# Kernel optimization log

Hardware: AMD Instinct MI355X
Metric: run time of the kernel (lower is better)

## Reference

```python
import jax, jax.numpy as jnp
import numpy as np

D_MODEL = 1792
BB = 256
I = D_MODEL + BB  # inner_dim = 2048


def setup_inputs() -> dict:
    key = jax.random.key(0)
    ks = jax.random.split(key, 10)
    s = 1.0 / np.sqrt(I)  # PyTorch LSTM default init range
    u = lambda k, shape: jax.random.uniform(k, shape, jnp.float32, -s, s)
    return {
        "x": jax.random.normal(ks[0], (6, D_MODEL), jnp.float32),
        "y": jax.random.normal(ks[1], (5, BB), jnp.float32),
        "Wih5": u(ks[2], (5, 4 * I, I)),
        "Whh5": u(ks[3], (5, 4 * I, I)),
        "bih5": u(ks[4], (5, 4 * I)),
        "bhh5": u(ks[5], (5, 4 * I)),
        "WihF": u(ks[6], (4 * I, D_MODEL)),
        "WhhF": u(ks[7], (4 * I, I)),
        "bihF": u(ks[8], (4 * I,)),
        "bhhF": u(ks[9], (4 * I,)),
    }


def _cell(h, c, xt, Wih, Whh, bih, bhh):
    # PyTorch LSTM cell: gates in i, f, g, o order
    g = Wih @ xt + bih + Whh @ h + bhh  # (4I,)
    i, f, gg, o = jnp.split(g, 4)
    c = jax.nn.sigmoid(f) * c + jax.nn.sigmoid(i) * jnp.tanh(gg)
    h = jax.nn.sigmoid(o) * jnp.tanh(c)
    return h, c


def reference(x, y, Wih5, Whh5, bih5, bhh5, WihF, WhhF, bihF, bhhF):
    # inpt: (5, inner_dim) = concat of first 5 frames and 5 gts
    inpt = jnp.concatenate([x[:-1], y], axis=1)
    h0 = jnp.zeros((I,), x.dtype)
    c0 = jnp.zeros((I,), x.dtype)

    def step(carry, xs):
        h, c = carry
        xt, Wih, Whh, bih, bhh = xs
        return _cell(h, c, xt, Wih, Whh, bih, bhh), None

    # 5 sequential single-step LSTM cells (distinct weights), fused via scan
    (h, c), _ = jax.lax.scan(step, (h0, c0), (inpt, Wih5, Whh5, bih5, bhh5))
    # final LSTM consumes the last frame (d_model input)
    h, c = _cell(h, c, x[-1], WihF, WhhF, bihF, bhhF)
    return h[-BB:]
```

## Files before the change

kernel.cpp:

```cpp
#include <hip/hip_runtime.h>
#include <cmath>

#define D_MODEL 1792
#define BB      256
#define II      2048
#define FOURI   8192

__device__ __forceinline__ float sigm(float v) { return 1.0f / (1.0f + expf(-v)); }

__device__ __forceinline__ float waveReduce(float s) {
    #pragma unroll
    for (int off = 32; off > 0; off >>= 1) s += __shfl_down(s, off, 64);
    return s;
}

__device__ __forceinline__ void stage2048(float* dst, const float* src, int tid) {
    float4* d4 = (float4*)dst;
    const float4* s4 = (const float4*)src;
    d4[tid]       = s4[tid];
    d4[tid + 256] = s4[tid + 256];
    __syncthreads();
}

__device__ __forceinline__ void stageConcat(float* dst, const float* xt,
                                            const float* yt, int tid) {
    float4* d4 = (float4*)dst;
    const float4* x4 = (const float4*)xt;
    const float4* y4 = (const float4*)yt;
    int i = tid;
    d4[i] = (i < 448) ? x4[i] : y4[i - 448];
    i = tid + 256;
    d4[i] = (i < 448) ? x4[i] : y4[i - 448];
    __syncthreads();
}

__device__ __forceinline__ float dotLds(const float* __restrict__ w,
                                        const float* hs, int lane) {
    float s = 0.f;
    #pragma unroll
    for (int p = 0; p < 8; ++p) {
        const int j = p * 256 + lane * 4;
        float4 a = *(const float4*)(w + j);
        float4 b = *(const float4*)(hs + j);
        s += a.x * b.x + a.y * b.y + a.z * b.z + a.w * b.w;
    }
    return s;
}

__global__ __launch_bounds__(256) void k0(
    const float* __restrict__ x, const float* __restrict__ y,
    const float* __restrict__ Wih5,
    const float* __restrict__ bih5, const float* __restrict__ bhh5,
    float* __restrict__ h0, float* __restrict__ c0, float* __restrict__ gih1)
{
    __shared__ float buf[II];
    __shared__ float partial[4];
    const int tid = threadIdx.x, wave = tid >> 6, lane = tid & 63;
    const int b = blockIdx.x;

    if (b < II) {
        stageConcat(buf, x, y, tid);
        if (wave != 1) {
            const float* wr = Wih5 + ((size_t)wave * II + b) * (size_t)II;
            float s = dotLds(wr, buf, lane);
            s = waveReduce(s);
            if (lane == 0)
                partial[wave] = s + bih5[wave * II + b] + bhh5[wave * II + b];
        } else {
            const float* wr = Wih5 + ((size_t)FOURI + b) * (size_t)II;
            const float* xt = x + D_MODEL;
            const float* yt = y + BB;
            float s = 0.f;
            #pragma unroll
            for (int p = 0; p < 8; ++p) {
                const int j = p * 256 + lane * 4;
                float4 a = *(const float4*)(wr + j);
                float4 v = (p < 7) ? *(const float4*)(xt + j)
                                   : *(const float4*)(yt + (j - D_MODEL));
                s += a.x * v.x + a.y * v.y + a.z * v.z + a.w * v.w;
            }
            s = waveReduce(s);
            if (lane == 0)
                gih1[b] = s + bih5[FOURI + b] + bhh5[FOURI + b];
        }
        __syncthreads();
        if (tid == 0) {
            const float cc = sigm(partial[0]) * tanhf(partial[2]);
            c0[b] = cc;
            h0[b] = sigm(partial[3]) * tanhf(cc);
        }
    } else {
        stageConcat(buf, x + D_MODEL, y + BB, tid);
        const int row = II + (b - II) * 4 + wave;
        const float* wr = Wih5 + ((size_t)FOURI + row) * (size_t)II;
        float s = dotLds(wr, buf, lane);
        s = waveReduce(s);
        if (lane == 0)
            gih1[row] = s + bih5[FOURI + row] + bhh5[FOURI + row];
    }
}

__global__ __launch_bounds__(256) void kmid(
    const float* __restrict__ Whh,
    const float* __restrict__ gih_t,
    const float* __restrict__ h_in, float* __restrict__ h_out,
    float* __restrict__ c,
    const float* __restrict__ WihN,
    const float* __restrict__ bihN, const float* __restrict__ bhhN,
    const float* __restrict__ xN, const float* __restrict__ yN,
    float* __restrict__ gihN)
{
    __shared__ float buf[II];
    __shared__ float partial[4];
    const int tid = threadIdx.x, wave = tid >> 6, lane = tid & 63;
    const int b = blockIdx.x;

    if (b < II) {
        stage2048(buf, h_in, tid);
        const float* wr = Whh + ((size_t)wave * II + b) * (size_t)II;
        float s = dotLds(wr, buf, lane);
        s = waveReduce(s);
        if (lane == 0) partial[wave] = s + gih_t[wave * II + b];
        __syncthreads();
        if (tid == 0) {
            const float cc = sigm(partial[1]) * c[b]
                           + sigm(partial[0]) * tanhf(partial[2]);
            c[b] = cc;
            h_out[b] = sigm(partial[3]) * tanhf(cc);
        }
    } else {
        stageConcat(buf, xN, yN, tid);
        const int row = (b - II) * 4 + wave;
        const float* wr = WihN + (size_t)row * (size_t)II;
        float s = dotLds(wr, buf, lane);
        s = waveReduce(s);
        if (lane == 0) gihN[row] = s + bihN[row] + bhhN[row];
    }
}

__global__ __launch_bounds__(256) void k4(
    const float* __restrict__ Whh4, const float* __restrict__ gih4,
    const float* __restrict__ h_in, float* __restrict__ h_out,
    float* __restrict__ c,
    const float* __restrict__ WihF, const float* __restrict__ bihF,
    const float* __restrict__ bhhF, const float* __restrict__ x5,
    float* __restrict__ gihF)
{
    __shared__ float buf[II];
    __shared__ float partial[4];
    const int tid = threadIdx.x, wave = tid >> 6, lane = tid & 63;
    const int b = blockIdx.x;

    if (b < II) {
        stage2048(buf, h_in, tid);
        const float* wr = Whh4 + ((size_t)wave * II + b) * (size_t)II;
        float s = dotLds(wr, buf, lane);
        s = waveReduce(s);
        if (lane == 0) partial[wave] = s + gih4[wave * II + b];
        __syncthreads();
        if (tid == 0) {
            const float cc = sigm(partial[1]) * c[b]
                           + sigm(partial[0]) * tanhf(partial[2]);
            c[b] = cc;
            h_out[b] = sigm(partial[3]) * tanhf(cc);
        }
    } else {
        float4* d4 = (float4*)buf;
        const float4* s4 = (const float4*)x5;
        d4[tid] = (tid < 448) ? s4[tid] : make_float4(0.f, 0.f, 0.f, 0.f);
        if (tid < 192) d4[tid + 256] = s4[tid + 256];
        __syncthreads();
        const int j = (b - II) * 4 + wave;
        const int row = (j >> 8) * II + D_MODEL + (j & 255);
        const float* wr = WihF + (size_t)row * (size_t)D_MODEL;
        float s = 0.f;
        #pragma unroll
        for (int p = 0; p < 7; ++p) {
            const int jj = p * 256 + lane * 4;
            float4 a = *(const float4*)(wr + jj);
            float4 v = *(const float4*)(buf + jj);
            s += a.x * v.x + a.y * v.y + a.z * v.z + a.w * v.w;
        }
        s = waveReduce(s);
        if (lane == 0) gihF[j] = s + bihF[row] + bhhF[row];
    }
}

__global__ __launch_bounds__(256) void k5(
    const float* __restrict__ WhhF, const float* __restrict__ gihF,
    const float* __restrict__ h_in, const float* __restrict__ c,
    float* __restrict__ out)
{
    __shared__ float buf[II];
    __shared__ float partial[4];
    const int tid = threadIdx.x, wave = tid >> 6, lane = tid & 63;
    const int b = blockIdx.x;

    stage2048(buf, h_in, tid);
    const int r = D_MODEL + b;
    const float* wr = WhhF + ((size_t)wave * II + r) * (size_t)II;
    float s = dotLds(wr, buf, lane);
    s = waveReduce(s);
    if (lane == 0) partial[wave] = s + gihF[wave * BB + b];
    __syncthreads();
    if (tid == 0) {
        const float cc = sigm(partial[1]) * c[r]
                       + sigm(partial[0]) * tanhf(partial[2]);
        out[b] = sigm(partial[3]) * tanhf(cc);
    }
}

extern "C" void kernel_launch(void* const* d_in, const int* in_sizes, int n_in,
                              void* d_out, int out_size, void* d_ws, size_t ws_size,
                              hipStream_t stream) {
    const float* x    = (const float*)d_in[0];
    const float* y    = (const float*)d_in[1];
    const float* Wih5 = (const float*)d_in[2];
    const float* Whh5 = (const float*)d_in[3];
    const float* bih5 = (const float*)d_in[4];
    const float* bhh5 = (const float*)d_in[5];
    const float* WihF = (const float*)d_in[6];
    const float* WhhF = (const float*)d_in[7];
    const float* bihF = (const float*)d_in[8];
    const float* bhhF = (const float*)d_in[9];
    float* out = (float*)d_out;

    float* ws   = (float*)d_ws;
    float* gihA = ws;
    float* gihB = gihA + FOURI;
    float* gihF = gihB + FOURI;
    float* hA   = gihF + 1024;
    float* hB   = hA + II;
    float* cbuf = hB + II;

    const size_t WOFF = (size_t)FOURI * II;

    k0<<<3584, 256, 0, stream>>>(x, y, Wih5, bih5, bhh5, hA, cbuf, gihA);

    kmid<<<4096, 256, 0, stream>>>(
        Whh5 + 1 * WOFF, gihA, hA, hB, cbuf,
        Wih5 + 2 * WOFF, bih5 + 2 * FOURI, bhh5 + 2 * FOURI,
        x + 2 * D_MODEL, y + 2 * BB, gihB);

    kmid<<<4096, 256, 0, stream>>>(
        Whh5 + 2 * WOFF, gihB, hB, hA, cbuf,
        Wih5 + 3 * WOFF, bih5 + 3 * FOURI, bhh5 + 3 * FOURI,
        x + 3 * D_MODEL, y + 3 * BB, gihA);

    kmid<<<4096, 256, 0, stream>>>(
        Whh5 + 3 * WOFF, gihA, hA, hB, cbuf,
        Wih5 + 4 * WOFF, bih5 + 4 * FOURI, bhh5 + 4 * FOURI,
        x + 4 * D_MODEL, y + 4 * BB, gihB);

    k4<<<2304, 256, 0, stream>>>(
        Whh5 + 4 * WOFF, gihB, hB, hA, cbuf,
        WihF, bihF, bhhF, x + 5 * D_MODEL, gihF);

    k5<<<BB, 256, 0, stream>>>(WhhF, gihF, hA, cbuf, out);
}
```

Before: 122.3 us.

## Drop LDS staging of vectors and merge next-step Wih rows into recurrent blocks

Vector operands (h, x/y concat) are now read directly from global memory instead of being staged into shared memory with a barrier, so the 8 KB LDS buffer goes away. Each block now does both its recurrent Whh gate rows and four Wih rows for the next step, which halves the grid to 2048 blocks per kernel. Each block does more work in exchange for fewer blocks and less LDS. The vector reads now go through the cache once per wave rather than once per block.

Measured after the change: 120.1 us. Within noise of the previous version (-1.8%).

```diff
diff --git a/kernel.cpp b/kernel.cpp
--- a/kernel.cpp
+++ b/kernel.cpp
@@ -5,6 +5,7 @@
 #define BB      256
 #define II      2048
 #define FOURI   8192
+#define G       2048
 
 __device__ __forceinline__ float sigm(float v) { return 1.0f / (1.0f + expf(-v)); }
 
@@ -14,93 +15,70 @@
     return s;
 }
 
-__device__ __forceinline__ void stage2048(float* dst, const float* src, int tid) {
-    float4* d4 = (float4*)dst;
-    const float4* s4 = (const float4*)src;
-    d4[tid]       = s4[tid];
-    d4[tid + 256] = s4[tid + 256];
-    __syncthreads();
-}
-
-__device__ __forceinline__ void stageConcat(float* dst, const float* xt,
-                                            const float* yt, int tid) {
-    float4* d4 = (float4*)dst;
-    const float4* x4 = (const float4*)xt;
-    const float4* y4 = (const float4*)yt;
-    int i = tid;
-    d4[i] = (i < 448) ? x4[i] : y4[i - 448];
-    i = tid + 256;
-    d4[i] = (i < 448) ? x4[i] : y4[i - 448];
-    __syncthreads();
-}
-
-__device__ __forceinline__ float dotLds(const float* __restrict__ w,
-                                        const float* hs, int lane) {
+__device__ __forceinline__ float dotG(const float* __restrict__ w,
+                                      const float* __restrict__ v, int lane) {
     float s = 0.f;
     #pragma unroll
     for (int p = 0; p < 8; ++p) {
         const int j = p * 256 + lane * 4;
         float4 a = *(const float4*)(w + j);
-        float4 b = *(const float4*)(hs + j);
+        float4 b = *(const float4*)(v + j);
         s += a.x * b.x + a.y * b.y + a.z * b.z + a.w * b.w;
     }
     return s;
 }
 
-__global__ __launch_bounds__(256) void k0(
+__device__ __forceinline__ float dotConcat(const float* __restrict__ w,
+                                           const float* __restrict__ xt,
+                                           const float* __restrict__ yt,
+                                           int lane) {
+    float s = 0.f;
+    #pragma unroll
+    for (int p = 0; p < 8; ++p) {
+        const int j = p * 256 + lane * 4;
+        float4 a = *(const float4*)(w + j);
+        float4 b = (p < 7) ? *(const float4*)(xt + j)
+                           : *(const float4*)(yt + (j - D_MODEL));
+        s += a.x * b.x + a.y * b.y + a.z * b.z + a.w * b.w;
+    }
+    return s;
+}
+
+__global__ __launch_bounds__(256) void k_first(
     const float* __restrict__ x, const float* __restrict__ y,
     const float* __restrict__ Wih5,
     const float* __restrict__ bih5, const float* __restrict__ bhh5,
     float* __restrict__ h0, float* __restrict__ c0, float* __restrict__ gih1)
 {
-    __shared__ float buf[II];
-    __shared__ float partial[4];
-    const int tid = threadIdx.x, wave = tid >> 6, lane = tid & 63;
-    const int b = blockIdx.x;
-
-    if (b < II) {
-        stageConcat(buf, x, y, tid);
-        if (wave != 1) {
-            const float* wr = Wih5 + ((size_t)wave * II + b) * (size_t)II;
-            float s = dotLds(wr, buf, lane);
-            s = waveReduce(s);
-            if (lane == 0)
-                partial[wave] = s + bih5[wave * II + b] + bhh5[wave * II + b];
-        } else {
-            const float* wr = Wih5 + ((size_t)FOURI + b) * (size_t)II;
-            const float* xt = x + D_MODEL;
-            const float* yt = y + BB;
-            float s = 0.f;
-            #pragma unroll
-            for (int p = 0; p < 8; ++p) {
-                const int j = p * 256 + lane * 4;
-                float4 a = *(const float4*)(wr + j);
-                float4 v = (p < 7) ? *(const float4*)(xt + j)
-                                   : *(const float4*)(yt + (j - D_MODEL));
-                s += a.x * v.x + a.y * v.y + a.z * v.z + a.w * v.w;
-            }
-            s = waveReduce(s);
-            if (lane == 0)
-                gih1[b] = s + bih5[FOURI + b] + bhh5[FOURI + b];
-        }
-        __syncthreads();
-        if (tid == 0) {
-            const float cc = sigm(partial[0]) * tanhf(partial[2]);
-            c0[b] = cc;
-            h0[b] = sigm(partial[3]) * tanhf(cc);
-        }
-    } else {
-        stageConcat(buf, x + D_MODEL, y + BB, tid);
-        const int row = II + (b - II) * 4 + wave;
+    __shared__ float partial[4];
+    const int tid = threadIdx.x, wave = tid >> 6, lane = tid & 63;
+    const int b = blockIdx.x;
+
+    if (wave != 1) {
+        const float* wr = Wih5 + ((size_t)wave * II + b) * (size_t)II;
+        float s = dotConcat(wr, x, y, lane);
+        s = waveReduce(s);
+        if (lane == 0)
+            partial[wave] = s + bih5[wave * II + b] + bhh5[wave * II + b];
+    }
+    __syncthreads();
+    if (tid == 0) {
+        const float cc = sigm(partial[0]) * tanhf(partial[2]);
+        c0[b] = cc;
+        h0[b] = sigm(partial[3]) * tanhf(cc);
+    }
+
+    {
+        const int row = b * 4 + wave;
         const float* wr = Wih5 + ((size_t)FOURI + row) * (size_t)II;
-        float s = dotLds(wr, buf, lane);
+        float s = dotConcat(wr, x + D_MODEL, y + BB, lane);
         s = waveReduce(s);
         if (lane == 0)
             gih1[row] = s + bih5[FOURI + row] + bhh5[FOURI + row];
     }
 }
 
-__global__ __launch_bounds__(256) void kmid(
+__global__ __launch_bounds__(256) void k_mid(
     const float* __restrict__ Whh,
     const float* __restrict__ gih_t,
     const float* __restrict__ h_in, float* __restrict__ h_out,
@@ -110,29 +88,28 @@
     const float* __restrict__ xN, const float* __restrict__ yN,
     float* __restrict__ gihN)
 {
-    __shared__ float buf[II];
-    __shared__ float partial[4];
-    const int tid = threadIdx.x, wave = tid >> 6, lane = tid & 63;
-    const int b = blockIdx.x;
-
-    if (b < II) {
-        stage2048(buf, h_in, tid);
+    __shared__ float partial[4];
+    const int tid = threadIdx.x, wave = tid >> 6, lane = tid & 63;
+    const int b = blockIdx.x;
+
+    {
         const float* wr = Whh + ((size_t)wave * II + b) * (size_t)II;
-        float s = dotLds(wr, buf, lane);
+        float s = dotG(wr, h_in, lane);
         s = waveReduce(s);
         if (lane == 0) partial[wave] = s + gih_t[wave * II + b];
-        __syncthreads();
-        if (tid == 0) {
-            const float cc = sigm(partial[1]) * c[b]
-                           + sigm(partial[0]) * tanhf(partial[2]);
-            c[b] = cc;
-            h_out[b] = sigm(partial[3]) * tanhf(cc);
-        }
-    } else {
-        stageConcat(buf, xN, yN, tid);
-        const int row = (b - II) * 4 + wave;
+    }
+    __syncthreads();
+    if (tid == 0) {
+        const float cc = sigm(partial[1]) * c[b]
+                       + sigm(partial[0]) * tanhf(partial[2]);
+        c[b] = cc;
+        h_out[b] = sigm(partial[3]) * tanhf(cc);
+    }
+
+    {
+        const int row = b * 4 + wave;
         const float* wr = WihN + (size_t)row * (size_t)II;
-        float s = dotLds(wr, buf, lane);
+        float s = dotConcat(wr, xN, yN, lane);
         s = waveReduce(s);
         if (lane == 0) gihN[row] = s + bihN[row] + bhhN[row];
     }
@@ -146,31 +123,26 @@
     const float* __restrict__ bhhF, const float* __restrict__ x5,
     float* __restrict__ gihF)
 {
-    __shared__ float buf[II];
-    __shared__ float partial[4];
-    const int tid = threadIdx.x, wave = tid >> 6, lane = tid & 63;
-    const int b = blockIdx.x;
-
-    if (b < II) {
-        stage2048(buf, h_in, tid);
+    __shared__ float partial[4];
+    const int tid = threadIdx.x, wave = tid >> 6, lane = tid & 63;
+    const int b = blockIdx.x;
+
+    {
         const float* wr = Whh4 + ((size_t)wave * II + b) * (size_t)II;
-        float s = dotLds(wr, buf, lane);
+        float s = dotG(wr, h_in, lane);
         s = waveReduce(s);
         if (lane == 0) partial[wave] = s + gih4[wave * II + b];
-        __syncthreads();
-        if (tid == 0) {
-            const float cc = sigm(partial[1]) * c[b]
-                           + sigm(partial[0]) * tanhf(partial[2]);
-            c[b] = cc;
-            h_out[b] = sigm(partial[3]) * tanhf(cc);
-        }
-    } else {
-        float4* d4 = (float4*)buf;
-        const float4* s4 = (const float4*)x5;
-        d4[tid] = (tid < 448) ? s4[tid] : make_float4(0.f, 0.f, 0.f, 0.f);
-        if (tid < 192) d4[tid + 256] = s4[tid + 256];
-        __syncthreads();
-        const int j = (b - II) * 4 + wave;
+    }
+    __syncthreads();
+    if (tid == 0) {
+        const float cc = sigm(partial[1]) * c[b]
+                       + sigm(partial[0]) * tanhf(partial[2]);
+        c[b] = cc;
+        h_out[b] = sigm(partial[3]) * tanhf(cc);
+    }
+
+    if (b < BB) {
+        const int j = b * 4 + wave;
         const int row = (j >> 8) * II + D_MODEL + (j & 255);
         const float* wr = WihF + (size_t)row * (size_t)D_MODEL;
         float s = 0.f;
@@ -178,7 +150,7 @@
         for (int p = 0; p < 7; ++p) {
             const int jj = p * 256 + lane * 4;
             float4 a = *(const float4*)(wr + jj);
-            float4 v = *(const float4*)(buf + jj);
+            float4 v = *(const float4*)(x5 + jj);
             s += a.x * v.x + a.y * v.y + a.z * v.z + a.w * v.w;
         }
         s = waveReduce(s);
@@ -191,15 +163,13 @@
     const float* __restrict__ h_in, const float* __restrict__ c,
     float* __restrict__ out)
 {
-    __shared__ float buf[II];
-    __shared__ float partial[4];
-    const int tid = threadIdx.x, wave = tid >> 6, lane = tid & 63;
-    const int b = blockIdx.x;
-
-    stage2048(buf, h_in, tid);
+    __shared__ float partial[4];
+    const int tid = threadIdx.x, wave = tid >> 6, lane = tid & 63;
+    const int b = blockIdx.x;
     const int r = D_MODEL + b;
+
     const float* wr = WhhF + ((size_t)wave * II + r) * (size_t)II;
-    float s = dotLds(wr, buf, lane);
+    float s = dotG(wr, h_in, lane);
     s = waveReduce(s);
     if (lane == 0) partial[wave] = s + gihF[wave * BB + b];
     __syncthreads();
@@ -235,24 +205,24 @@
 
     const size_t WOFF = (size_t)FOURI * II;
 
-    k0<<<3584, 256, 0, stream>>>(x, y, Wih5, bih5, bhh5, hA, cbuf, gihA);
-
-    kmid<<<4096, 256, 0, stream>>>(
+    k_first<<<G, 256, 0, stream>>>(x, y, Wih5, bih5, bhh5, hA, cbuf, gihA);
+
+    k_mid<<<G, 256, 0, stream>>>(
         Whh5 + 1 * WOFF, gihA, hA, hB, cbuf,
         Wih5 + 2 * WOFF, bih5 + 2 * FOURI, bhh5 + 2 * FOURI,
         x + 2 * D_MODEL, y + 2 * BB, gihB);
 
-    kmid<<<4096, 256, 0, stream>>>(
+    k_mid<<<G, 256, 0, stream>>>(
         Whh5 + 2 * WOFF, gihB, hB, hA, cbuf,
         Wih5 + 3 * WOFF, bih5 + 3 * FOURI, bhh5 + 3 * FOURI,
         x + 3 * D_MODEL, y + 3 * BB, gihA);
 
-    kmid<<<4096, 256, 0, stream>>>(
+    k_mid<<<G, 256, 0, stream>>>(
         Whh5 + 3 * WOFF, gihA, hA, hB, cbuf,
         Wih5 + 4 * WOFF, bih5 + 4 * FOURI, bhh5 + 4 * FOURI,
         x + 4 * D_MODEL, y + 4 * BB, gihB);
 
-    k4<<<2304, 256, 0, stream>>>(
+    k4<<<G, 256, 0, stream>>>(
         Whh5 + 4 * WOFF, gihB, hB, hA, cbuf,
         WihF, bihF, bhhF, x + 5 * D_MODEL, gihF);
 
```
